# Performance work log

Hardware: AMD Instinct MI355X
Metric: run time of the kernel (lower is better)

Reference implementation:

```python
import jax, jax.numpy as jnp
import numpy as np

N_NODES = 100000


def _gcn_conv(x, W, b, src, dst, num_nodes):
    # x: [N, Fin] -> h: [N, Fout]
    h = x @ W
    # symmetric normalization deg^-1/2[src] * deg^-1/2[dst] (self-loops already appended)
    ones = jnp.ones(src.shape[0], dtype=x.dtype)
    deg = jax.ops.segment_sum(ones, dst, num_segments=num_nodes)
    dinv = jnp.where(deg > 0, jax.lax.rsqrt(deg), 0.0)
    norm = dinv[src] * dinv[dst]  # [E]
    msg = h[src] * norm[:, None]  # [E, Fout] -- dominant memory traffic
    out = jax.ops.segment_sum(msg, dst, num_segments=num_nodes)
    return out + b


def setup_inputs() -> dict:
    key = jax.random.key(0)
    ks = jax.random.split(key, 8)
    N, F_IN, H = N_NODES, 128, 64
    E = 3200000
    x = jax.random.normal(ks[0], (N, F_IN), dtype=jnp.float32)
    edge_index = jax.random.randint(ks[1], (2, E), 0, N, dtype=jnp.int64)
    s1 = 1.0 / np.sqrt(F_IN)
    s2 = 1.0 / np.sqrt(H)
    return {
        "x": x,
        "edge_index": edge_index,
        "W1": jax.random.normal(ks[2], (F_IN, H), dtype=jnp.float32) * s1,
        "b1": jnp.zeros((H,), dtype=jnp.float32),
        "W2": jax.random.normal(ks[3], (H, H), dtype=jnp.float32) * s2,
        "b2": jnp.zeros((H,), dtype=jnp.float32),
        "W_time": jax.random.normal(ks[4], (H, 1), dtype=jnp.float32) * s2,
        "b_time": jnp.zeros((1,), dtype=jnp.float32),
        "W_event": jax.random.normal(ks[5], (H, 1), dtype=jnp.float32) * s2,
        "b_event": jnp.zeros((1,), dtype=jnp.float32),
    }


def reference(x, edge_index, W1, b1, W2, b2, W_time, b_time, W_event, b_event):
    N = x.shape[0]
    # GCNConv default: add self-loops before normalization/aggregation
    loops = jnp.arange(N, dtype=edge_index.dtype)
    src = jnp.concatenate([edge_index[0], loops])
    dst = jnp.concatenate([edge_index[1], loops])

    h = jax.nn.relu(_gcn_conv(x, W1, b1, src, dst, N))
    # dropout is identity in eval mode
    h = jax.nn.relu(_gcn_conv(h, W2, b2, src, dst, N))

    survival_time = h @ W_time + b_time    # [N, 1]
    event_status = h @ W_event + b_event   # [N, 1]
    return survival_time, event_status
```

## Files before the change

kernel.cpp:

```cpp
#include <hip/hip_runtime.h>
#include <math.h>

constexpr int H = 64;
constexpr int FIN = 128;
constexpr int BIN_SHIFT = 8;
constexpr int BIN_NODES = 1 << BIN_SHIFT;
constexpr int MAX_BINS = 512;
constexpr int BIN_CAP = 10240;
constexpr int SRC_BITS = 24;
constexpr unsigned SRC_MASK = (1u << SRC_BITS) - 1;
constexpr int KB_TPB = 512;
constexpr int KB_BLOCKS = 512;
constexpr int KB_ITER = 13;

typedef __attribute__((ext_vector_type(8))) __bf16 bf16x8;
typedef __attribute__((ext_vector_type(4))) float f32x4;
typedef __attribute__((ext_vector_type(2))) float f32x2;

__device__ inline float bf2f(unsigned short u) {
    unsigned v = ((unsigned)u) << 16;
    return __builtin_bit_cast(float, v);
}
__device__ inline unsigned short f2bf(float f) {
    unsigned u = __builtin_bit_cast(unsigned, f);
    unsigned rnd = 0x7FFFu + ((u >> 16) & 1u);
    return (unsigned short)((u + rnd) >> 16);
}
__device__ inline float bflo(unsigned u) { return __builtin_bit_cast(float, u << 16); }
__device__ inline float bfhi(unsigned u) { return __builtin_bit_cast(float, u & 0xFFFF0000u); }

__device__ inline int wave_incl_scan(int v, int lane) {
#pragma unroll
    for (int off = 1; off < 64; off <<= 1) {
        int t = __shfl_up(v, off);
        if (lane >= off) v += t;
    }
    return v;
}

__global__ void k_initcur(int* __restrict__ cursor, int nbins) {
    int i = blockIdx.x * blockDim.x + threadIdx.x;
    if (i < nbins) cursor[i] = i * BIN_CAP;
}

__global__ __launch_bounds__(512) void k_bin(
    const int* __restrict__ src, const int* __restrict__ dst, int E, int nbins,
    int* __restrict__ cursor, int* __restrict__ binned) {
    __shared__ int hist[MAX_BINS];
    __shared__ int base[MAX_BINS];
    __shared__ int loff[MAX_BINS];
    __shared__ int words[KB_ITER * KB_TPB];
    __shared__ int wsum[8];
    int tid = threadIdx.x, lane = tid & 63, wid = tid >> 6;
    long long e0 = (long long)E * blockIdx.x / gridDim.x;
    long long e1 = (long long)E * (blockIdx.x + 1) / gridDim.x;
    int chunk = (int)(e1 - e0);
    for (int i = tid; i < MAX_BINS; i += KB_TPB) hist[i] = 0;
    __syncthreads();
    int packed[KB_ITER];
#pragma unroll
    for (int i = 0; i < KB_ITER; ++i) {
        int o = i * KB_TPB + tid;
        packed[i] = -1;
        if (o < chunk) {
            int d = dst[e0 + o];
            int b = d >> BIN_SHIFT;
            int r = atomicAdd(&hist[b], 1);
            packed[i] = (b << 22) | ((d & (BIN_NODES - 1)) << 14) | r;
        }
    }
    __syncthreads();
    {
        int c0 = hist[tid];
        int incl = wave_incl_scan(c0, lane);
        if (lane == 63) wsum[wid] = incl;
        __syncthreads();
        int woff = 0;
        for (int w = 0; w < wid; ++w) woff += wsum[w];
        int ex = woff + incl - c0;
        loff[tid] = ex;
        if (tid < nbins && c0) base[tid] = atomicAdd(&cursor[tid], c0);
    }
    __syncthreads();
#pragma unroll
    for (int i = 0; i < KB_ITER; ++i) {
        int o = i * KB_TPB + tid;
        if (o < chunk) {
            unsigned w = (unsigned)packed[i];
            int b = (int)(w >> 22);
            int dl = (int)((w >> 14) & 0xFF);
            int r = (int)(w & 0x3FFF);
            words[loff[b] + r] = (int)(((unsigned)dl << SRC_BITS) | (unsigned)src[e0 + o]);
        }
    }
    __syncthreads();
    for (int b = tid; b < nbins; b += KB_TPB) {
        int n = hist[b];
        if (!n) continue;
        int g = base[b];
        int l = loff[b];
        int i = 0;
        while (i < n && ((g + i) & 3)) { binned[g + i] = words[l + i]; ++i; }
        for (; i + 4 <= n; i += 4) {
            int4 v = make_int4(words[l + i], words[l + i + 1], words[l + i + 2], words[l + i + 3]);
            *(int4*)&binned[g + i] = v;
        }
        for (; i < n; ++i) binned[g + i] = words[l + i];
    }
    for (int o = KB_ITER * KB_TPB + tid; o < chunk; o += KB_TPB) {
        int d = dst[e0 + o];
        int b = d >> BIN_SHIFT;
        int r = atomicAdd(&cursor[b], 1);
        binned[r] = (int)(((unsigned)(d & (BIN_NODES - 1)) << SRC_BITS) | (unsigned)src[e0 + o]);
    }
}

__global__ __launch_bounds__(256) void k_binscan(
    const int* __restrict__ cursor, int nbins,
    int* __restrict__ binbase, int* __restrict__ rowptr, int N, int E) {
    __shared__ int wsum[4];
    int tid = threadIdx.x, lane = tid & 63, wid = tid >> 6;
    int b0 = tid * 4;
    int c[4];
#pragma unroll
    for (int k = 0; k < 4; ++k) {
        int b = b0 + k;
        c[k] = (b < nbins) ? cursor[b] - b * BIN_CAP : 0;
    }
    int t = c[0] + c[1] + c[2] + c[3];
    int incl = wave_incl_scan(t, lane);
    if (lane == 63) wsum[wid] = incl;
    __syncthreads();
    int woff = 0;
    for (int w = 0; w < wid; ++w) woff += wsum[w];
    int p = woff + incl - t;
#pragma unroll
    for (int k = 0; k < 4; ++k) {
        int b = b0 + k;
        if (b < nbins) binbase[b] = p;
        p += c[k];
    }
    if (tid == 0) rowptr[N] = E;
}

__global__ __launch_bounds__(512) void k_binsort(
    const int* __restrict__ cursor, const int* __restrict__ binbase,
    const int* __restrict__ binned, int N,
    int* __restrict__ csr_src, int* __restrict__ rowptr, float* __restrict__ dinv) {
    __shared__ int cnt[BIN_NODES];
    __shared__ int excl[BIN_NODES];
    __shared__ int rnk[BIN_NODES];
    __shared__ int wsum[4];
    int bin = blockIdx.x;
    int tid = threadIdx.x, lane = tid & 63, wid = tid >> 6;
    int n = cursor[bin] - bin * BIN_CAP;
    int gbase = binbase[bin];
    const int* bp = binned + (size_t)bin * BIN_CAP;
    if (tid < BIN_NODES) { cnt[tid] = 0; rnk[tid] = 0; }
    __syncthreads();
    for (int i = tid; i < n; i += 512)
        atomicAdd(&cnt[((unsigned)bp[i]) >> SRC_BITS], 1);
    __syncthreads();
    int v = 0, incl = 0;
    if (tid < BIN_NODES) {
        v = cnt[tid];
        incl = wave_incl_scan(v, lane);
        if (lane == 63) wsum[wid] = incl;
    }
    __syncthreads();
    if (tid < BIN_NODES) {
        int woff = 0;
        for (int w = 0; w < wid; ++w) woff += wsum[w];
        int ex = woff + incl - v;
        excl[tid] = ex;
        int node = bin * BIN_NODES + tid;
        if (node < N) {
            rowptr[node] = gbase + ex;
            dinv[node] = 1.0f / sqrtf((float)v + 1.0f);
        }
    }
    __syncthreads();
    for (int i = tid; i < n; i += 512) {
        unsigned w = (unsigned)bp[i];
        int dl = w >> SRC_BITS;
        int r = atomicAdd(&rnk[dl], 1);
        csr_src[gbase + excl[dl] + r] = (int)(w & SRC_MASK);
    }
}

template<int K, bool RELU_IN>
__global__ __launch_bounds__(256) void k_mgemm(
    const float* __restrict__ X, const float* __restrict__ W,
    const float* __restrict__ bias, const float* __restrict__ dinv,
    int N, unsigned short* __restrict__ A16) {
    constexpr int LDK = K + 8;
    __shared__ short sX[64 * LDK];
    __shared__ short sWt[64 * LDK];
    int tid = threadIdx.x;
    for (int idx = tid; idx < K * 64; idx += 256) {
        int k = idx >> 6, c = idx & 63;
        sWt[c * LDK + k] = (short)f2bf(W[idx]);
    }
    {
        int row = tid >> 2;
        int q0 = (tid & 3) * (K / 4);
        int grow = blockIdx.x * 64 + row;
        const float* xp = X + (size_t)grow * K + q0;
        unsigned* dstp = (unsigned*)&sX[row * LDK + q0];
#pragma unroll
        for (int i = 0; i < K / 16; ++i) {
            float4 v = make_float4(0.f, 0.f, 0.f, 0.f);
            if (grow < N) v = *(const float4*)(xp + i * 4);
            if (RELU_IN) {
                float4 bb = *(const float4*)(bias + q0 + i * 4);
                v.x = fmaxf(v.x + bb.x, 0.f); v.y = fmaxf(v.y + bb.y, 0.f);
                v.z = fmaxf(v.z + bb.z, 0.f); v.w = fmaxf(v.w + bb.w, 0.f);
            }
            unsigned lo = (unsigned)f2bf(v.x) | ((unsigned)f2bf(v.y) << 16);
            unsigned hi = (unsigned)f2bf(v.z) | ((unsigned)f2bf(v.w) << 16);
            dstp[i * 2] = lo;
            dstp[i * 2 + 1] = hi;
        }
    }
    __syncthreads();
    int w = tid >> 6, lane = tid & 63;
    int mrow = lane & 15, kgrp = lane >> 4;
    f32x4 acc[4] = {};
    const short* xbase = &sX[(16 * w + mrow) * LDK + kgrp * 8];
    const short* wbase = &sWt[mrow * LDK + kgrp * 8];
#pragma unroll
    for (int t = 0; t < K / 32; ++t) {
        bf16x8 a = *(const bf16x8*)(xbase + 32 * t);
#pragma unroll
        for (int c = 0; c < 4; ++c) {
            bf16x8 b = *(const bf16x8*)(wbase + 16 * c * LDK + 32 * t);
            acc[c] = __builtin_amdgcn_mfma_f32_16x16x32_bf16(a, b, acc[c], 0, 0, 0);
        }
    }
    int r0g = blockIdx.x * 64 + 16 * w + kgrp * 4;
#pragma unroll
    for (int r = 0; r < 4; ++r) {
        int rg = r0g + r;
        if (rg < N) {
            float dv = dinv[rg];
#pragma unroll
            for (int c = 0; c < 4; ++c)
                A16[(size_t)rg * H + 16 * c + mrow] = f2bf(acc[c][r] * dv);
        }
    }
}

__device__ inline void acc8(f32x2* acc, uint4 u) {
    f32x2 v0 = {bflo(u.x), bfhi(u.x)};
    f32x2 v1 = {bflo(u.y), bfhi(u.y)};
    f32x2 v2 = {bflo(u.z), bfhi(u.z)};
    f32x2 v3 = {bflo(u.w), bfhi(u.w)};
    acc[0] += v0; acc[1] += v1; acc[2] += v2; acc[3] += v3;
}

template<bool FUSE>
__global__ __launch_bounds__(256) void k_gather(
    const int* __restrict__ rowptr, const int* __restrict__ csr_src,
    const float* __restrict__ dinv, const unsigned short* __restrict__ A16,
    float* __restrict__ B, int N,
    const float* __restrict__ b2, const float* __restrict__ Wt, const float* __restrict__ bt,
    const float* __restrict__ We, const float* __restrict__ be, float* __restrict__ out) {
    int w = threadIdx.x >> 6;
    int lane = threadIdx.x & 63;
    int grp = lane >> 3, sub = lane & 7;
    const uint4* A8 = (const uint4*)A16;
    int nodeA = blockIdx.x * 8 + w;
    int nodeB = nodeA + 4;
    int begA = 0, endA = 0, begB = 0, endB = 0;
    if (nodeA < N) { begA = rowptr[nodeA]; endA = rowptr[nodeA + 1]; }
    if (nodeB < N) { begB = rowptr[nodeB]; endB = rowptr[nodeB + 1]; }
    int mA0 = endA - begA; if (mA0 > 64) mA0 = 64;
    int mB0 = endB - begB; if (mB0 > 64) mB0 = 64;
    int idA = (lane < mA0) ? csr_src[begA + lane] : 0;
    int idB = (lane < mB0) ? csr_src[begB + lane] : 0;
    f32x2 aA[4] = {}, aB[4] = {};
    if (grp == 0 && nodeA < N) acc8(aA, A8[(size_t)nodeA * 8 + sub]);
    if (grp == 0 && nodeB < N) acc8(aB, A8[(size_t)nodeB * 8 + sub]);

    auto gather_node = [&](int beg, int end, int idFirst, f32x2* acc) {
        f32x2 t[4] = {};
        for (int e0 = beg; e0 < end; e0 += 64) {
            int m = end - e0; if (m > 64) m = 64;
            int id = (e0 == beg) ? idFirst : ((lane < m) ? csr_src[e0 + lane] : 0);
            int c = 0;
            for (; c + 16 <= m; c += 16) {
                int s0 = __shfl(id, c + grp);
                int s1 = __shfl(id, c + 8 + grp);
                uint4 u0 = A8[(size_t)s0 * 8 + sub];
                uint4 u1 = A8[(size_t)s1 * 8 + sub];
                acc8(acc, u0);
                acc8(t, u1);
            }
            for (; c < m; c += 8) {
                int cc = c + grp;
                int s = __shfl(id, cc < m ? cc : 0);
                if (cc < m) acc8(acc, A8[(size_t)s * 8 + sub]);
            }
        }
#pragma unroll
        for (int j = 0; j < 4; ++j) acc[j] += t[j];
    };
    gather_node(begA, endA, idA, aA);
    gather_node(begB, endB, idB, aB);

#pragma unroll
    for (int off = 8; off < 64; off <<= 1) {
#pragma unroll
        for (int j = 0; j < 4; ++j) {
            aA[j][0] += __shfl_xor(aA[j][0], off);
            aA[j][1] += __shfl_xor(aA[j][1], off);
            aB[j][0] += __shfl_xor(aB[j][0], off);
            aB[j][1] += __shfl_xor(aB[j][1], off);
        }
    }
    if (grp == 0) {
#pragma unroll
        for (int which = 0; which < 2; ++which) {
            int node = which ? nodeB : nodeA;
            if (node >= N) continue;
            f32x2* a = which ? aB : aA;
            float dv = dinv[node];
            float r[8];
#pragma unroll
            for (int j = 0; j < 4; ++j) { r[2 * j] = a[j][0] * dv; r[2 * j + 1] = a[j][1] * dv; }
            if (!FUSE) {
                float* bp = B + (size_t)node * H + sub * 8;
                *(float4*)bp = make_float4(r[0], r[1], r[2], r[3]);
                *(float4*)(bp + 4) = make_float4(r[4], r[5], r[6], r[7]);
            } else {
                int f = sub * 8;
                float p1 = 0.f, p2 = 0.f;
#pragma unroll
                for (int j = 0; j < 8; ++j) {
                    float g = fmaxf(r[j] + b2[f + j], 0.f);
                    p1 += g * Wt[f + j];
                    p2 += g * We[f + j];
                }
#pragma unroll
                for (int off = 1; off < 8; off <<= 1) {
                    p1 += __shfl_xor(p1, off);
                    p2 += __shfl_xor(p2, off);
                }
                if (sub == 0) {
                    out[node] = p1 + bt[0];
                    out[N + node] = p2 + be[0];
                }
            }
        }
    }
}

extern "C" void kernel_launch(void* const* d_in, const int* in_sizes, int n_in,
                              void* d_out, int out_size, void* d_ws, size_t ws_size,
                              hipStream_t stream) {
    const float* x  = (const float*)d_in[0];
    const int* edge = (const int*)d_in[1];
    const float* W1 = (const float*)d_in[2];
    const float* b1 = (const float*)d_in[3];
    const float* W2 = (const float*)d_in[4];
    const float* b2 = (const float*)d_in[5];
    const float* Wt = (const float*)d_in[6];
    const float* bt = (const float*)d_in[7];
    const float* We = (const float*)d_in[8];
    const float* be = (const float*)d_in[9];

    int N = in_sizes[0] / FIN;
    int E = in_sizes[1] / 2;
    const int* src = edge;
    const int* dst = edge + E;
    int nbins = (N + BIN_NODES - 1) >> BIN_SHIFT;

    char* ws = (char*)d_ws;
    size_t off = 0;
    auto alloc = [&](size_t bytes) {
        void* p = ws + off;
        off += (bytes + 255) & ~size_t(255);
        return p;
    };
    float* dinv    = (float*)alloc((size_t)N * sizeof(float));
    int*   rowptr  = (int*)alloc((size_t)(N + 1) * sizeof(int));
    int*   cursor  = (int*)alloc((size_t)nbins * sizeof(int));
    int*   binbase = (int*)alloc((size_t)nbins * sizeof(int));
    int*   binned  = (int*)alloc((size_t)nbins * BIN_CAP * sizeof(int));
    int*   csr_src = (int*)alloc((size_t)E * sizeof(int));
    unsigned short* A16 = (unsigned short*)alloc((size_t)N * H * sizeof(unsigned short));
    float* B       = (float*)alloc((size_t)N * H * sizeof(float));

    k_initcur<<<(nbins + 255) / 256, 256, 0, stream>>>(cursor, nbins);
    k_bin<<<KB_BLOCKS, KB_TPB, 0, stream>>>(src, dst, E, nbins, cursor, binned);
    k_binscan<<<1, 256, 0, stream>>>(cursor, nbins, binbase, rowptr, N, E);
    k_binsort<<<nbins, 512, 0, stream>>>(cursor, binbase, binned, N, csr_src, rowptr, dinv);

    int ggrid = (N + 63) / 64;
    k_mgemm<FIN, false><<<ggrid, 256, 0, stream>>>(x, W1, nullptr, dinv, N, A16);
    k_gather<false><<<(N + 7) / 8, 256, 0, stream>>>(rowptr, csr_src, dinv, A16, B, N,
                                                     nullptr, nullptr, nullptr, nullptr, nullptr, nullptr);

    k_mgemm<H, true><<<ggrid, 256, 0, stream>>>(B, W2, b1, dinv, N, A16);
    k_gather<true><<<(N + 7) / 8, 256, 0, stream>>>(rowptr, csr_src, dinv, A16, nullptr, N,
                                                    b2, Wt, bt, We, be, (float*)d_out);
}
```

Before: 215.7 us.

## Fuse bias+ReLU into gather, store bf16 intermediate, fold bin scan into binsort

The first gather now applies bias and ReLU and writes a bf16 intermediate instead of fp32, so the second GEMM loads bf16 directly and skips conversion. The cursor init kernel becomes a memset, and the standalone bin scan kernel is removed: each binsort block recomputes the prefix over bin counts itself. This cuts intermediate memory traffic and two launches, at the cost of redundant scans per block.

```diff
diff --git a/kernel.cpp b/kernel.cpp
--- a/kernel.cpp
+++ b/kernel.cpp
@@ -17,10 +17,6 @@
 typedef __attribute__((ext_vector_type(4))) float f32x4;
 typedef __attribute__((ext_vector_type(2))) float f32x2;
 
-__device__ inline float bf2f(unsigned short u) {
-    unsigned v = ((unsigned)u) << 16;
-    return __builtin_bit_cast(float, v);
-}
 __device__ inline unsigned short f2bf(float f) {
     unsigned u = __builtin_bit_cast(unsigned, f);
     unsigned rnd = 0x7FFFu + ((u >> 16) & 1u);
@@ -38,14 +34,9 @@
     return v;
 }
 
-__global__ void k_initcur(int* __restrict__ cursor, int nbins) {
-    int i = blockIdx.x * blockDim.x + threadIdx.x;
-    if (i < nbins) cursor[i] = i * BIN_CAP;
-}
-
 __global__ __launch_bounds__(512) void k_bin(
     const int* __restrict__ src, const int* __restrict__ dst, int E, int nbins,
-    int* __restrict__ cursor, int* __restrict__ binned) {
+    int* __restrict__ gcnt, int* __restrict__ binned) {
     __shared__ int hist[MAX_BINS];
     __shared__ int base[MAX_BINS];
     __shared__ int loff[MAX_BINS];
@@ -77,9 +68,8 @@
         __syncthreads();
         int woff = 0;
         for (int w = 0; w < wid; ++w) woff += wsum[w];
-        int ex = woff + incl - c0;
-        loff[tid] = ex;
-        if (tid < nbins && c0) base[tid] = atomicAdd(&cursor[tid], c0);
+        loff[tid] = woff + incl - c0;
+        if (tid < nbins && c0) base[tid] = tid * BIN_CAP + atomicAdd(&gcnt[tid], c0);
     }
     __syncthreads();
 #pragma unroll
@@ -110,54 +100,35 @@
     for (int o = KB_ITER * KB_TPB + tid; o < chunk; o += KB_TPB) {
         int d = dst[e0 + o];
         int b = d >> BIN_SHIFT;
-        int r = atomicAdd(&cursor[b], 1);
+        int r = b * BIN_CAP + atomicAdd(&gcnt[b], 1);
         binned[r] = (int)(((unsigned)(d & (BIN_NODES - 1)) << SRC_BITS) | (unsigned)src[e0 + o]);
     }
 }
 
-__global__ __launch_bounds__(256) void k_binscan(
-    const int* __restrict__ cursor, int nbins,
-    int* __restrict__ binbase, int* __restrict__ rowptr, int N, int E) {
-    __shared__ int wsum[4];
-    int tid = threadIdx.x, lane = tid & 63, wid = tid >> 6;
-    int b0 = tid * 4;
-    int c[4];
-#pragma unroll
-    for (int k = 0; k < 4; ++k) {
-        int b = b0 + k;
-        c[k] = (b < nbins) ? cursor[b] - b * BIN_CAP : 0;
-    }
-    int t = c[0] + c[1] + c[2] + c[3];
-    int incl = wave_incl_scan(t, lane);
-    if (lane == 63) wsum[wid] = incl;
-    __syncthreads();
-    int woff = 0;
-    for (int w = 0; w < wid; ++w) woff += wsum[w];
-    int p = woff + incl - t;
-#pragma unroll
-    for (int k = 0; k < 4; ++k) {
-        int b = b0 + k;
-        if (b < nbins) binbase[b] = p;
-        p += c[k];
-    }
-    if (tid == 0) rowptr[N] = E;
-}
-
 __global__ __launch_bounds__(512) void k_binsort(
-    const int* __restrict__ cursor, const int* __restrict__ binbase,
-    const int* __restrict__ binned, int N,
+    const int* __restrict__ gcnt, const int* __restrict__ binned, int N, int E, int nbins,
     int* __restrict__ csr_src, int* __restrict__ rowptr, float* __restrict__ dinv) {
+    __shared__ int binex[MAX_BINS];
     __shared__ int cnt[BIN_NODES];
     __shared__ int excl[BIN_NODES];
     __shared__ int rnk[BIN_NODES];
-    __shared__ int wsum[4];
+    __shared__ int wsum[8];
     int bin = blockIdx.x;
     int tid = threadIdx.x, lane = tid & 63, wid = tid >> 6;
-    int n = cursor[bin] - bin * BIN_CAP;
-    int gbase = binbase[bin];
+    {
+        int v = (tid < nbins) ? gcnt[tid] : 0;
+        int incl = wave_incl_scan(v, lane);
+        if (lane == 63) wsum[wid] = incl;
+        __syncthreads();
+        int woff = 0;
+        for (int w = 0; w < wid; ++w) woff += wsum[w];
+        binex[tid] = woff + incl - v;
+    }
+    if (tid < BIN_NODES) { cnt[tid] = 0; rnk[tid] = 0; }
+    __syncthreads();
+    int n = gcnt[bin];
+    int gbase = binex[bin];
     const int* bp = binned + (size_t)bin * BIN_CAP;
-    if (tid < BIN_NODES) { cnt[tid] = 0; rnk[tid] = 0; }
-    __syncthreads();
     for (int i = tid; i < n; i += 512)
         atomicAdd(&cnt[((unsigned)bp[i]) >> SRC_BITS], 1);
     __syncthreads();
@@ -179,6 +150,7 @@
             dinv[node] = 1.0f / sqrtf((float)v + 1.0f);
         }
     }
+    if (bin == 0 && tid == 0) rowptr[N] = E;
     __syncthreads();
     for (int i = tid; i < n; i += 512) {
         unsigned w = (unsigned)bp[i];
@@ -188,11 +160,10 @@
     }
 }
 
-template<int K, bool RELU_IN>
+template<int K, bool BF16_IN>
 __global__ __launch_bounds__(256) void k_mgemm(
-    const float* __restrict__ X, const float* __restrict__ W,
-    const float* __restrict__ bias, const float* __restrict__ dinv,
-    int N, unsigned short* __restrict__ A16) {
+    const void* __restrict__ Xv, const float* __restrict__ W,
+    const float* __restrict__ dinv, int N, unsigned short* __restrict__ A16) {
     constexpr int LDK = K + 8;
     __shared__ short sX[64 * LDK];
     __shared__ short sWt[64 * LDK];
@@ -201,7 +172,21 @@
         int k = idx >> 6, c = idx & 63;
         sWt[c * LDK + k] = (short)f2bf(W[idx]);
     }
-    {
+    if constexpr (BF16_IN) {
+        const unsigned short* Xs = (const unsigned short*)Xv;
+        int row = tid >> 2, q0 = (tid & 3) * 16;
+        int grow = blockIdx.x * 64 + row;
+        uint4 u0 = make_uint4(0, 0, 0, 0), u1 = u0;
+        if (grow < N) {
+            const uint4* xp = (const uint4*)(Xs + (size_t)grow * K + q0);
+            u0 = xp[0];
+            u1 = xp[1];
+        }
+        uint4* dp = (uint4*)&sX[row * LDK + q0];
+        dp[0] = u0;
+        dp[1] = u1;
+    } else {
+        const float* X = (const float*)Xv;
         int row = tid >> 2;
         int q0 = (tid & 3) * (K / 4);
         int grow = blockIdx.x * 64 + row;
@@ -211,11 +196,6 @@
         for (int i = 0; i < K / 16; ++i) {
             float4 v = make_float4(0.f, 0.f, 0.f, 0.f);
             if (grow < N) v = *(const float4*)(xp + i * 4);
-            if (RELU_IN) {
-                float4 bb = *(const float4*)(bias + q0 + i * 4);
-                v.x = fmaxf(v.x + bb.x, 0.f); v.y = fmaxf(v.y + bb.y, 0.f);
-                v.z = fmaxf(v.z + bb.z, 0.f); v.w = fmaxf(v.w + bb.w, 0.f);
-            }
             unsigned lo = (unsigned)f2bf(v.x) | ((unsigned)f2bf(v.y) << 16);
             unsigned hi = (unsigned)f2bf(v.z) | ((unsigned)f2bf(v.w) << 16);
             dstp[i * 2] = lo;
@@ -262,8 +242,8 @@
 __global__ __launch_bounds__(256) void k_gather(
     const int* __restrict__ rowptr, const int* __restrict__ csr_src,
     const float* __restrict__ dinv, const unsigned short* __restrict__ A16,
-    float* __restrict__ B, int N,
-    const float* __restrict__ b2, const float* __restrict__ Wt, const float* __restrict__ bt,
+    unsigned short* __restrict__ X2, int N,
+    const float* __restrict__ bias, const float* __restrict__ Wt, const float* __restrict__ bt,
     const float* __restrict__ We, const float* __restrict__ be, float* __restrict__ out) {
     int w = threadIdx.x >> 6;
     int lane = threadIdx.x & 63;
@@ -328,16 +308,17 @@
             float r[8];
 #pragma unroll
             for (int j = 0; j < 4; ++j) { r[2 * j] = a[j][0] * dv; r[2 * j + 1] = a[j][1] * dv; }
+            int f = sub * 8;
             if (!FUSE) {
-                float* bp = B + (size_t)node * H + sub * 8;
-                *(float4*)bp = make_float4(r[0], r[1], r[2], r[3]);
-                *(float4*)(bp + 4) = make_float4(r[4], r[5], r[6], r[7]);
+                unsigned short o[8];
+#pragma unroll
+                for (int j = 0; j < 8; ++j) o[j] = f2bf(fmaxf(r[j] + bias[f + j], 0.f));
+                *(uint4*)(X2 + (size_t)node * H + f) = *(uint4*)o;
             } else {
-                int f = sub * 8;
                 float p1 = 0.f, p2 = 0.f;
 #pragma unroll
                 for (int j = 0; j < 8; ++j) {
-                    float g = fmaxf(r[j] + b2[f + j], 0.f);
+                    float g = fmaxf(r[j] + bias[f + j], 0.f);
                     p1 += g * Wt[f + j];
                     p2 += g * We[f + j];
                 }
@@ -384,24 +365,22 @@
     };
     float* dinv    = (float*)alloc((size_t)N * sizeof(float));
     int*   rowptr  = (int*)alloc((size_t)(N + 1) * sizeof(int));
-    int*   cursor  = (int*)alloc((size_t)nbins * sizeof(int));
-    int*   binbase = (int*)alloc((size_t)nbins * sizeof(int));
+    int*   gcnt    = (int*)alloc((size_t)nbins * sizeof(int));
     int*   binned  = (int*)alloc((size_t)nbins * BIN_CAP * sizeof(int));
     int*   csr_src = (int*)alloc((size_t)E * sizeof(int));
     unsigned short* A16 = (unsigned short*)alloc((size_t)N * H * sizeof(unsigned short));
-    float* B       = (float*)alloc((size_t)N * H * sizeof(float));
-
-    k_initcur<<<(nbins + 255) / 256, 256, 0, stream>>>(cursor, nbins);
-    k_bin<<<KB_BLOCKS, KB_TPB, 0, stream>>>(src, dst, E, nbins, cursor, binned);
-    k_binscan<<<1, 256, 0, stream>>>(cursor, nbins, binbase, rowptr, N, E);
-    k_binsort<<<nbins, 512, 0, stream>>>(cursor, binbase, binned, N, csr_src, rowptr, dinv);
+    unsigned short* X2  = (unsigned short*)alloc((size_t)N * H * sizeof(unsigned short));
+
+    hipMemsetAsync(gcnt, 0, (size_t)nbins * sizeof(int), stream);
+    k_bin<<<KB_BLOCKS, KB_TPB, 0, stream>>>(src, dst, E, nbins, gcnt, binned);
+    k_binsort<<<nbins, 512, 0, stream>>>(gcnt, binned, N, E, nbins, csr_src, rowptr, dinv);
 
     int ggrid = (N + 63) / 64;
-    k_mgemm<FIN, false><<<ggrid, 256, 0, stream>>>(x, W1, nullptr, dinv, N, A16);
-    k_gather<false><<<(N + 7) / 8, 256, 0, stream>>>(rowptr, csr_src, dinv, A16, B, N,
-                                                     nullptr, nullptr, nullptr, nullptr, nullptr, nullptr);
-
-    k_mgemm<H, true><<<ggrid, 256, 0, stream>>>(B, W2, b1, dinv, N, A16);
+    k_mgemm<FIN, false><<<ggrid, 256, 0, stream>>>(x, W1, dinv, N, A16);
+    k_gather<false><<<(N + 7) / 8, 256, 0, stream>>>(rowptr, csr_src, dinv, A16, X2, N,
+                                                     b1, nullptr, nullptr, nullptr, nullptr, nullptr);
+
+    k_mgemm<H, true><<<ggrid, 256, 0, stream>>>(X2, W2, dinv, N, A16);
     k_gather<true><<<(N + 7) / 8, 256, 0, stream>>>(rowptr, csr_src, dinv, A16, nullptr, N,
                                                     b2, Wt, bt, We, be, (float*)d_out);
 }
```

Result: no change. 217.1 us (median of 2 runs) (+0.7%).
